# Performance work log

Measured on AMD Instinct MI355X. Metric: run time of the kernel, lower is better.

Reference implementation:

```python
import jax, jax.numpy as jnp
import numpy as np

N, E, G = 10000, 160000, 64     # nodes, edges, graphs in batch
T, F_IN, F_OUT, L = 5, 75, 15, 4  # towers, per-tower in (divide_input=False), per-tower out, conv layers
AVG_DEG_LOG = float(np.log(17.0))  # stand-in for PyG histogram stat (source deg=zeros -> NaN)
BN_EPS = 1e-5
STD_EPS = 1e-5


def _u(key, shape):
    fi, fo = shape[-2], shape[-1]
    lim = float(np.sqrt(6.0 / (fi + fo)))
    return jax.random.uniform(key, shape, jnp.float32, -lim, lim)


def setup_inputs():
    key = jax.random.key(0)
    k = iter(jax.random.split(key, 24))
    inp = {}
    inp["x"] = jax.random.randint(next(k), (N, 2), 0, 21)
    inp["edge_index"] = jax.random.randint(next(k), (2, E), 0, N)
    inp["edge_attr"] = jax.random.randint(next(k), (E, 2), 0, 4)
    inp["batch"] = jnp.sort(jax.random.randint(next(k), (N,), 0, G))
    inp["node_emb"] = jax.random.normal(next(k), (21, 75), jnp.float32)
    inp["edge_emb"] = jax.random.normal(next(k), (4, 25), jnp.float32)
    inp["pre_lin_W"] = _u(next(k), (150, 75)); inp["pre_lin_b"] = jnp.zeros((75,), jnp.float32)
    inp["edge_enc_W"] = _u(next(k), (L, 50, F_IN)); inp["edge_enc_b"] = jnp.zeros((L, F_IN), jnp.float32)
    inp["pre_W"] = _u(next(k), (L, T, 3 * F_IN, F_IN)); inp["pre_b"] = jnp.zeros((L, T, F_IN), jnp.float32)
    inp["post_W"] = _u(next(k), (L, T, 13 * F_IN, F_OUT)); inp["post_b"] = jnp.zeros((L, T, F_OUT), jnp.float32)
    inp["lin_W"] = _u(next(k), (L, T * F_OUT, 75)); inp["lin_b"] = jnp.zeros((L, 75), jnp.float32)
    inp["bn_g"] = jnp.ones((L, 75), jnp.float32); inp["bn_b"] = jnp.zeros((L, 75), jnp.float32)
    inp["mlp_W1"] = _u(next(k), (75, 50)); inp["mlp_b1"] = jnp.zeros((50,), jnp.float32)
    inp["mlp_W2"] = _u(next(k), (50, 25)); inp["mlp_b2"] = jnp.zeros((25,), jnp.float32)
    inp["mlp_W3"] = _u(next(k), (25, 1)); inp["mlp_b3"] = jnp.zeros((1,), jnp.float32)
    return inp


def _forward(x, edge_index, edge_attr, batch, node_emb, edge_emb, pre_lin_W, pre_lin_b,
             edge_enc_W, edge_enc_b, pre_W, pre_b, post_W, post_b, lin_W, lin_b,
             bn_g, bn_b, mlp_W1, mlp_b1, mlp_W2, mlp_b2, mlp_W3, mlp_b3):
    # node / edge embeddings -> features
    h = node_emb[x].reshape(N, 150) @ pre_lin_W + pre_lin_b          # [N,75]
    ea = edge_emb[edge_attr].reshape(E, 50)                           # [E,50]
    src, dst = edge_index[0], edge_index[1]  # messages flow src -> dst (x_j=src, x_i=dst)

    cnt = jax.ops.segment_sum(jnp.ones((E,), jnp.float32), dst, num_segments=N)  # in-degree [N]
    deg = jnp.maximum(cnt, 1.0)[:, None, None]
    log_deg = jnp.log(jnp.maximum(cnt, 1.0) + 1.0)[:, None, None]
    amp = log_deg / AVG_DEG_LOG
    att = AVG_DEG_LOG / log_deg
    has = (cnt > 0)[:, None, None]

    for l in range(L):
        e = ea @ edge_enc_W[l] + edge_enc_b[l]                        # [E,75]
        m_in = jnp.concatenate([h[dst], h[src], e], axis=-1)          # [E,225]
        msgs = jnp.einsum('ec,tcf->etf', m_in, pre_W[l]) + pre_b[l]   # [E,T,75]
        s = jax.ops.segment_sum(msgs, dst, num_segments=N)
        mean = s / deg
        mean_sq = jax.ops.segment_sum(msgs * msgs, dst, num_segments=N) / deg
        std = jnp.sqrt(jax.nn.relu(mean_sq - mean * mean) + STD_EPS)
        mn = jnp.where(has, jax.ops.segment_min(msgs, dst, num_segments=N), 0.0)
        mx = jnp.where(has, jax.ops.segment_max(msgs, dst, num_segments=N), 0.0)
        agg = jnp.concatenate([mean, mn, mx, std], axis=-1)           # [N,T,300]
        scaled = jnp.concatenate([agg, agg * amp, agg * att], axis=-1)  # [N,T,900]
        out = jnp.concatenate([jnp.broadcast_to(h[:, None, :], (N, T, F_IN)), scaled], axis=-1)  # [N,T,975]
        post = jnp.einsum('ntc,tcf->ntf', out, post_W[l]) + post_b[l]  # [N,T,15]
        hc = post.reshape(N, T * F_OUT) @ lin_W[l] + lin_b[l]          # [N,75]
        mu = hc.mean(axis=0)
        var = hc.var(axis=0)  # biased, matches BatchNorm1d training mode
        h = jax.nn.relu((hc - mu) / jnp.sqrt(var + BN_EPS) * bn_g[l] + bn_b[l])

    g = jax.ops.segment_sum(h, batch, num_segments=G)                 # global_add_pool [G,75]
    g = jax.nn.relu(g @ mlp_W1 + mlp_b1)
    g = jax.nn.relu(g @ mlp_W2 + mlp_b2)
    return g @ mlp_W3 + mlp_b3                                        # [G,1]


def reference(x, edge_index, edge_attr, batch, node_emb, edge_emb, pre_lin_W, pre_lin_b,
              edge_enc_W, edge_enc_b, pre_W, pre_b, post_W, post_b, lin_W, lin_b,
              bn_g, bn_b, mlp_W1, mlp_b1, mlp_W2, mlp_b2, mlp_W3, mlp_b3):
    return _forward(x, edge_index, edge_attr, batch, node_emb, edge_emb, pre_lin_W, pre_lin_b,
                    edge_enc_W, edge_enc_b, pre_W, pre_b, post_W, post_b, lin_W, lin_b,
                    bn_g, bn_b, mlp_W1, mlp_b1, mlp_W2, mlp_b2, mlp_W3, mlp_b3)
```

## Files before the change

kernel.cpp:

```cpp
#include <hip/hip_runtime.h>
#include <hip/hip_bf16.h>
#include <math.h>

#define NN 10000
#define NE 160000
#define NG 64
#define NT 5
#define NL 4
#define ADL 2.833213344056216f

#define OFF_H      0
#define OFF_HC     750000
#define OFF_P      1500000
#define OFF_Q      5250000
#define OFF_AGG    9000000
#define OFF_RLUT   24000000
#define OFF_INVDEG 24006000
#define OFF_AMP    24016000
#define OFF_ATT    24026000
#define OFF_STATS  24036000
#define OFF_GPOOL  24036160
#define OFF_INT    24118960

__device__ __forceinline__ float bf2f(__hip_bfloat16 v){ return __bfloat162float(v); }

__global__ void k_zero_cnt(int* cnt){
    int i = blockIdx.x*256 + threadIdx.x;
    if (i < NN) cnt[i] = 0;
}

__global__ __launch_bounds__(256) void k_h0(const int* __restrict__ x,
        const float* __restrict__ node_emb, const float* __restrict__ plW,
        const float* __restrict__ plb, float* __restrict__ h){
    __shared__ float s_emb[21*75];
    __shared__ float s_W[150*75];
    __shared__ float s_b[75];
    int tid = threadIdx.x;
    for (int i = tid; i < 21*75; i += 256) s_emb[i] = node_emb[i];
    for (int i = tid; i < 150*75; i += 256) s_W[i] = plW[i];
    if (tid < 75) s_b[tid] = plb[tid];
    __syncthreads();
    for (int out = blockIdx.x*256 + tid; out < NN*75; out += gridDim.x*256){
        int n = out / 75, f = out - n*75;
        int x0 = x[2*n], x1 = x[2*n+1];
        float acc = s_b[f];
        const float* e0 = s_emb + x0*75;
        const float* e1 = s_emb + x1*75;
        #pragma unroll 5
        for (int k = 0; k < 75; k++)
            acc += e0[k]*s_W[k*75+f] + e1[k]*s_W[(75+k)*75+f];
        h[out] = acc;
    }
}

__global__ void k_hist(const int* __restrict__ ei, int* __restrict__ cnt){
    int e = blockIdx.x*256 + threadIdx.x;
    if (e < NE) atomicAdd(&cnt[ei[NE + e]], 1);
}

__global__ void k_scan(const int* __restrict__ cnt, int* __restrict__ eoff){
    __shared__ int buf[256];
    __shared__ int carry;
    int tid = threadIdx.x;
    if (tid == 0){ carry = 0; eoff[0] = 0; }
    __syncthreads();
    for (int base = 0; base < NN; base += 256){
        int v = (base + tid < NN) ? cnt[base + tid] : 0;
        buf[tid] = v; __syncthreads();
        for (int off = 1; off < 256; off <<= 1){
            int t2 = (tid >= off) ? buf[tid - off] : 0;
            __syncthreads();
            buf[tid] += t2;
            __syncthreads();
        }
        int inc = buf[tid] + carry;
        if (base + tid < NN) eoff[base + tid + 1] = inc;
        __syncthreads();
        if (tid == 255) carry = inc;
        __syncthreads();
    }
}

__global__ void k_nodestats(const int* __restrict__ cnt, const int* __restrict__ eoff,
        float* __restrict__ invdeg, float* __restrict__ amp, float* __restrict__ att,
        int* __restrict__ cursor){
    int n = blockIdx.x*256 + threadIdx.x;
    if (n >= NN) return;
    int c = cnt[n];
    cursor[n] = eoff[n];
    float cf = (float)c;
    float dg = cf < 1.f ? 1.f : cf;
    invdeg[n] = 1.f / dg;
    float ld = logf(dg + 1.f);
    amp[n] = ld / ADL;
    att[n] = ADL / ld;
}

__global__ void k_scatter(const int* __restrict__ ei, const int* __restrict__ ea,
        int* __restrict__ cursor, int* __restrict__ esrc, int* __restrict__ ecombo){
    int e = blockIdx.x*256 + threadIdx.x;
    if (e >= NE) return;
    int src = ei[e], dst = ei[NE + e];
    int pos = atomicAdd(&cursor[dst], 1);
    esrc[pos] = src;
    ecombo[pos] = ea[2*e]*4 + ea[2*e+1];
}

__global__ __launch_bounds__(384) void k_pq(const float* __restrict__ h,
        const float* __restrict__ preW, const float* __restrict__ preb,
        const float* __restrict__ edge_emb, const float* __restrict__ encW,
        const float* __restrict__ encb, int l,
        __hip_bfloat16* __restrict__ P, __hip_bfloat16* __restrict__ Q,
        float* __restrict__ Rlut, float* __restrict__ stats){
    __shared__ float smem[10675];
    int tid = threadIdx.x;
    int bx = blockIdx.x;

    if (bx == 318){
        for (int i = tid; i < 150; i += 384) stats[i] = 0.f;
        return;
    }
    if (bx >= 313){
        int t = bx - 313;
        float* s_encW = smem;
        float* s_ev   = smem + 3750;
        float* s_wc   = smem + 4950;
        float* s_ee   = smem + 10575;
        for (int i = tid; i < 3750; i += 384) s_encW[i] = encW[(size_t)l*3750 + i];
        for (int i = tid; i < 100; i += 384) s_ee[i] = edge_emb[i];
        const float* wcsrc = preW + (((size_t)(l*NT + t))*225 + 150)*75;
        for (int i = tid; i < 5625; i += 384) s_wc[i] = wcsrc[i];
        __syncthreads();
        for (int task = tid; task < 1200; task += 384){
            int b = task/75, m = task - 75*b;
            int a0 = b >> 2, a1 = b & 3;
            float s = encb[l*75 + m];
            for (int k = 0; k < 25; k++)
                s += s_ee[a0*25+k]*s_encW[k*75+m] + s_ee[a1*25+k]*s_encW[(25+k)*75+m];
            s_ev[task] = s;
        }
        __syncthreads();
        for (int task = tid; task < 1200; task += 384){
            int b = task/75, f = task - 75*b;
            float r = preb[((size_t)l*NT + t)*75 + f];
            const float* ev = s_ev + b*75;
            #pragma unroll 5
            for (int m = 0; m < 75; m++) r += ev[m]*s_wc[m*75 + f];
            Rlut[b*375 + t*75 + f] = r;
        }
        return;
    }

    float* h_t = smem;
    int base = bx*32;
    for (int idx = tid; idx < 32*75; idx += 384){
        int i = idx/75, m = idx - 75*i;
        int n = base + i;
        h_t[i*76 + m] = (n < NN) ? h[(size_t)n*75 + m] : 0.f;
    }
    __syncthreads();
    int j = tid;
    if (j >= 375) return;
    int t = j/75, f = j - 75*t;
    const float* wbase = preW + ((size_t)(l*NT + t))*225*75 + f;
    float accP[32], accQ[32];
    #pragma unroll
    for (int i = 0; i < 32; i++){ accP[i] = 0.f; accQ[i] = 0.f; }
    for (int m = 0; m < 72; m += 4){
        float wa0 = wbase[(m+0)*75], wa1 = wbase[(m+1)*75];
        float wa2 = wbase[(m+2)*75], wa3 = wbase[(m+3)*75];
        float wb0 = wbase[(75+m+0)*75], wb1 = wbase[(75+m+1)*75];
        float wb2 = wbase[(75+m+2)*75], wb3 = wbase[(75+m+3)*75];
        #pragma unroll
        for (int i = 0; i < 32; i++){
            const float4 hv = *(const float4*)&h_t[i*76 + m];
            accP[i] += hv.x*wa0 + hv.y*wa1 + hv.z*wa2 + hv.w*wa3;
            accQ[i] += hv.x*wb0 + hv.y*wb1 + hv.z*wb2 + hv.w*wb3;
        }
    }
    for (int m = 72; m < 75; m++){
        float wa = wbase[m*75], wb = wbase[(75+m)*75];
        #pragma unroll
        for (int i = 0; i < 32; i++){
            float v = h_t[i*76 + m];
            accP[i] += v*wa; accQ[i] += v*wb;
        }
    }
    for (int i = 0; i < 32; i++){
        int n = base + i;
        if (n < NN){
            P[(size_t)n*375 + j] = __float2bfloat16(accP[i]);
            Q[(size_t)n*375 + j] = __float2bfloat16(accQ[i]);
        }
    }
}

__global__ __launch_bounds__(64) void k_agg(const __hip_bfloat16* __restrict__ P,
        const __hip_bfloat16* __restrict__ Q, const float* __restrict__ Rlut,
        const int* __restrict__ eoff, const int* __restrict__ esrc,
        const int* __restrict__ ecombo, const float* __restrict__ invdeg,
        __hip_bfloat16* __restrict__ agg){
    int n = blockIdx.y;
    int j = blockIdx.x*64 + threadIdx.x;
    if (j >= 375) return;
    int lo = eoff[n], hi = eoff[n+1];
    float p = bf2f(P[(size_t)n*375 + j]);
    float sum = 0.f, sq = 0.f, mn = 3.4e38f, mx = -3.4e38f;
    int e = lo;
    for (; e + 8 <= hi; e += 8){
        int s0 = esrc[e],   s1 = esrc[e+1], s2 = esrc[e+2], s3 = esrc[e+3];
        int s4 = esrc[e+4], s5 = esrc[e+5], s6 = esrc[e+6], s7 = esrc[e+7];
        int c0 = ecombo[e],   c1 = ecombo[e+1], c2 = ecombo[e+2], c3 = ecombo[e+3];
        int c4 = ecombo[e+4], c5 = ecombo[e+5], c6 = ecombo[e+6], c7 = ecombo[e+7];
        float q0 = bf2f(Q[(size_t)s0*375 + j]);
        float q1 = bf2f(Q[(size_t)s1*375 + j]);
        float q2 = bf2f(Q[(size_t)s2*375 + j]);
        float q3 = bf2f(Q[(size_t)s3*375 + j]);
        float q4 = bf2f(Q[(size_t)s4*375 + j]);
        float q5 = bf2f(Q[(size_t)s5*375 + j]);
        float q6 = bf2f(Q[(size_t)s6*375 + j]);
        float q7 = bf2f(Q[(size_t)s7*375 + j]);
        float r0 = Rlut[c0*375 + j], r1 = Rlut[c1*375 + j];
        float r2 = Rlut[c2*375 + j], r3 = Rlut[c3*375 + j];
        float r4 = Rlut[c4*375 + j], r5 = Rlut[c5*375 + j];
        float r6 = Rlut[c6*375 + j], r7 = Rlut[c7*375 + j];
        float m0 = p + q0 + r0, m1 = p + q1 + r1;
        float m2 = p + q2 + r2, m3 = p + q3 + r3;
        float m4 = p + q4 + r4, m5 = p + q5 + r5;
        float m6 = p + q6 + r6, m7 = p + q7 + r7;
        sum += (m0 + m1 + m2 + m3) + (m4 + m5 + m6 + m7);
        sq  += (m0*m0 + m1*m1 + m2*m2 + m3*m3) + (m4*m4 + m5*m5 + m6*m6 + m7*m7);
        mn = fminf(mn, fminf(fminf(fminf(m0,m1), fminf(m2,m3)),
                             fminf(fminf(m4,m5), fminf(m6,m7))));
        mx = fmaxf(mx, fmaxf(fmaxf(fmaxf(m0,m1), fmaxf(m2,m3)),
                             fmaxf(fmaxf(m4,m5), fmaxf(m6,m7))));
    }
    for (; e < hi; e++){
        int s = esrc[e], cm = ecombo[e];
        float m = p + bf2f(Q[(size_t)s*375 + j]) + Rlut[cm*375 + j];
        sum += m; sq += m*m;
        mn = fminf(mn, m); mx = fmaxf(mx, m);
    }
    float id = invdeg[n];
    bool has = hi > lo;
    float mean = sum*id;
    float msq  = sq*id;
    float var = msq - mean*mean; var = var > 0.f ? var : 0.f;
    float sd = sqrtf(var + 1e-5f);
    float mnv = has ? mn : 0.f;
    float mxv = has ? mx : 0.f;
    int t = j/75, f = j - 75*t;
    __hip_bfloat16* a = agg + ((size_t)n*NT + t)*300;
    a[f]      = __float2bfloat16(mean);
    a[75+f]   = __float2bfloat16(mnv);
    a[150+f]  = __float2bfloat16(mxv);
    a[225+f]  = __float2bfloat16(sd);
}

#define KB2 50
__global__ __launch_bounds__(256, 6) void k_post(const float* __restrict__ h,
        const __hip_bfloat16* __restrict__ agg, const float* __restrict__ postW,
        const float* __restrict__ postb, const float* __restrict__ amp,
        const float* __restrict__ att, int l, float* __restrict__ postbase){
    __shared__ float s_w[3*KB2*16];
    int t = blockIdx.y;
    int z = blockIdx.z;
    int nbase = blockIdx.x*256;
    int tid = threadIdx.x;
    int fg  = (tid & 3)*4;
    int sub = tid >> 2;
    const float* Wt = postW + ((size_t)(l*NT + t))*975*15;

    if (z == 0){
        for (int idx = tid; idx < 75*16; idx += 256){
            int c = idx >> 4, f = idx & 15;
            s_w[idx] = (f < 15) ? Wt[c*15 + f] : 0.f;
        }
        __syncthreads();
        float a1[4][4] = {};
        const float* hrow[4];
        #pragma unroll
        for (int j = 0; j < 4; j++){
            int n = nbase + sub + 64*j;
            hrow[j] = h + (size_t)(n < NN ? n : 0)*75;
        }
        #pragma unroll 3
        for (int k = 0; k < 75; k++){
            const float4 w1 = *(const float4*)&s_w[k*16 + fg];
            #pragma unroll
            for (int j = 0; j < 4; j++){
                float v = hrow[j][k];
                a1[j][0] += v*w1.x; a1[j][1] += v*w1.y;
                a1[j][2] += v*w1.z; a1[j][3] += v*w1.w;
            }
        }
        const float* pb = postb + (l*NT + t)*15;
        #pragma unroll
        for (int j = 0; j < 4; j++){
            int n = nbase + sub + 64*j;
            if (n >= NN) continue;
            float* dst = postbase + (size_t)n*75 + t*15;
            #pragma unroll
            for (int f = 0; f < 4; f++)
                if (fg + f < 15) dst[fg + f] = a1[j][f] + pb[fg + f];
        }
        return;
    }

    int kbeg = (z-1)*KB2;
    for (int idx = tid; idx < 3*KB2*16; idx += 256){
        int vrow = idx / (KB2*16);
        int rem = idx - vrow*(KB2*16);
        int c = rem >> 4, f = rem & 15;
        s_w[idx] = (f < 15) ? Wt[(75 + vrow*300 + kbeg + c)*15 + f] : 0.f;
    }
    __syncthreads();
    float a1[4][4] = {}, a2[4][4] = {}, a3[4][4] = {};
    const __hip_bfloat16* arow[4];
    #pragma unroll
    for (int j = 0; j < 4; j++){
        int n = nbase + sub + 64*j;
        arow[j] = agg + (size_t)(n < NN ? n : 0)*1500 + t*300 + kbeg;
    }
    #pragma unroll 2
    for (int k = 0; k < KB2; k++){
        const float4 w1 = *(const float4*)&s_w[k*16 + fg];
        const float4 w2 = *(const float4*)&s_w[(KB2 + k)*16 + fg];
        const float4 w3 = *(const float4*)&s_w[(2*KB2 + k)*16 + fg];
        #pragma unroll
        for (int j = 0; j < 4; j++){
            float v = bf2f(arow[j][k]);
            a1[j][0] += v*w1.x; a1[j][1] += v*w1.y;
            a1[j][2] += v*w1.z; a1[j][3] += v*w1.w;
            a2[j][0] += v*w2.x; a2[j][1] += v*w2.y;
            a2[j][2] += v*w2.z; a2[j][3] += v*w2.w;
            a3[j][0] += v*w3.x; a3[j][1] += v*w3.y;
            a3[j][2] += v*w3.z; a3[j][3] += v*w3.w;
        }
    }
    float* postv = postbase + (size_t)z*750000;
    #pragma unroll
    for (int j = 0; j < 4; j++){
        int n = nbase + sub + 64*j;
        if (n >= NN) continue;
        float am = amp[n], at = att[n];
        float* dst = postv + (size_t)n*75 + t*15;
        #pragma unroll
        for (int f = 0; f < 4; f++)
            if (fg + f < 15)
                dst[fg + f] = a1[j][f] + am*a2[j][f] + at*a3[j][f];
    }
}

__global__ __launch_bounds__(256) void k_lin(const float* __restrict__ postbase,
        const float* __restrict__ linW, const float* __restrict__ linb,
        int l, float* __restrict__ hc, float* __restrict__ stats){
    __shared__ float p_l[32*75];
    __shared__ float w_l[75*75];
    __shared__ float hc_l[32*75];
    int tid = threadIdx.x;
    int base = blockIdx.x*32;
    for (int i = tid; i < 75*75; i += 256) w_l[i] = linW[(size_t)l*5625 + i];
    for (int i = tid; i < 32*75; i += 256){
        int n = base + i/75;
        size_t idx = (size_t)base*75 + i;
        float v = 0.f;
        if (n < NN){
            #pragma unroll
            for (int z = 0; z < 7; z++) v += postbase[idx + (size_t)z*750000];
        }
        p_l[i] = v;
    }
    __syncthreads();
    for (int task = tid; task < 2400; task += 256){
        int i = task/75, o = task - 75*i;
        float s = linb[l*75 + o];
        const float* pl = p_l + i*75;
        #pragma unroll 5
        for (int j = 0; j < 75; j++) s += pl[j]*w_l[j*75 + o];
        hc_l[task] = s;
        if (base + i < NN) hc[(size_t)(base+i)*75 + o] = s;
    }
    __syncthreads();
    if (tid < 75){
        int nv = NN - base; if (nv > 32) nv = 32;
        float s1 = 0.f, s2 = 0.f;
        for (int i = 0; i < nv; i++){
            float v = hc_l[i*75 + tid];
            s1 += v; s2 += v*v;
        }
        atomicAdd(&stats[tid], s1);
        atomicAdd(&stats[75+tid], s2);
    }
}

__global__ void k_bnapply(const float* __restrict__ hc, const float* __restrict__ stats,
        const float* __restrict__ bng, const float* __restrict__ bnb, int l,
        float* __restrict__ h){
    int idx = blockIdx.x*256 + threadIdx.x;
    if (idx >= NN*75) return;
    int col = idx % 75;
    float mu = stats[col]*(1.0f/NN);
    float var = stats[75+col]*(1.0f/NN) - mu*mu;
    float inv = rsqrtf(var + 1e-5f);
    float v = (hc[idx] - mu)*inv*bng[l*75+col] + bnb[l*75+col];
    h[idx] = v > 0.f ? v : 0.f;
}

__global__ __launch_bounds__(256) void k_pool(const float* __restrict__ h,
        const int* __restrict__ batch, float* __restrict__ gpool){
    int g = blockIdx.x, tid = threadIdx.x;
    int lo = 0, hi = NN;
    while (lo < hi){ int mid = (lo+hi)>>1; if (batch[mid] < g) lo = mid+1; else hi = mid; }
    int start = lo;
    lo = start; hi = NN;
    while (lo < hi){ int mid = (lo+hi)>>1; if (batch[mid] < g+1) lo = mid+1; else hi = mid; }
    int end = lo;
    __shared__ float red[225];
    if (tid < 225){
        int col = tid % 75, rep = tid / 75;
        float acc = 0.f;
        for (int i = start + rep; i < end; i += 3) acc += h[(size_t)i*75 + col];
        red[tid] = acc;
    }
    __syncthreads();
    if (tid < 75) gpool[g*75 + tid] = red[tid] + red[75+tid] + red[150+tid];
}

__global__ __launch_bounds__(256) void k_mlp(const float* __restrict__ gpool,
        const float* __restrict__ W1, const float* __restrict__ b1,
        const float* __restrict__ W2, const float* __restrict__ b2,
        const float* __restrict__ W3, const float* __restrict__ b3,
        float* __restrict__ out){
    __shared__ float w1[75*50];
    __shared__ float w2[50*25];
    __shared__ float gp[8*75];
    __shared__ float t1[8*50];
    __shared__ float t2[8*25];
    int tid = threadIdx.x;
    int gbase = blockIdx.x*8;
    for (int i = tid; i < 75*50; i += 256) w1[i] = W1[i];
    for (int i = tid; i < 50*25; i += 256) w2[i] = W2[i];
    for (int i = tid; i < 8*75; i += 256) gp[i] = gpool[gbase*75 + i];
    __syncthreads();
    for (int task = tid; task < 8*50; task += 256){
        int g = task/50, j = task - 50*g;
        float s = b1[j];
        const float* gv = gp + g*75;
        #pragma unroll 5
        for (int k = 0; k < 75; k++) s += gv[k]*w1[k*50+j];
        t1[task] = s > 0.f ? s : 0.f;
    }
    __syncthreads();
    for (int task = tid; task < 8*25; task += 256){
        int g = task/25, j = task - 25*g;
        float s = b2[j];
        const float* tv = t1 + g*50;
        #pragma unroll 5
        for (int k = 0; k < 50; k++) s += tv[k]*w2[k*25+j];
        t2[task] = s > 0.f ? s : 0.f;
    }
    __syncthreads();
    if (tid < 8){
        float s = b3[0];
        const float* tv = t2 + tid*25;
        #pragma unroll
        for (int k = 0; k < 25; k++) s += tv[k]*W3[k];
        out[gbase + tid] = s;
    }
}

extern "C" void kernel_launch(void* const* d_in, const int* in_sizes, int n_in,
                              void* d_out, int out_size, void* d_ws, size_t ws_size,
                              hipStream_t stream){
    const int* x          = (const int*)d_in[0];
    const int* edge_index = (const int*)d_in[1];
    const int* edge_attr  = (const int*)d_in[2];
    const int* batch      = (const int*)d_in[3];
    const float* node_emb = (const float*)d_in[4];
    const float* edge_emb = (const float*)d_in[5];
    const float* pre_lin_W= (const float*)d_in[6];
    const float* pre_lin_b= (const float*)d_in[7];
    const float* encW     = (const float*)d_in[8];
    const float* encb     = (const float*)d_in[9];
    const float* preW     = (const float*)d_in[10];
    const float* preb     = (const float*)d_in[11];
    const float* postW    = (const float*)d_in[12];
    const float* postb    = (const float*)d_in[13];
    const float* linW     = (const float*)d_in[14];
    const float* linb     = (const float*)d_in[15];
    const float* bng      = (const float*)d_in[16];
    const float* bnb      = (const float*)d_in[17];
    const float* mlpW1    = (const float*)d_in[18];
    const float* mlpb1    = (const float*)d_in[19];
    const float* mlpW2    = (const float*)d_in[20];
    const float* mlpb2    = (const float*)d_in[21];
    const float* mlpW3    = (const float*)d_in[22];
    const float* mlpb3    = (const float*)d_in[23];

    float* ws = (float*)d_ws;
    float* h      = ws + OFF_H;
    float* hc     = ws + OFF_HC;
    __hip_bfloat16* P = (__hip_bfloat16*)(ws + OFF_P);
    __hip_bfloat16* Q = (__hip_bfloat16*)(ws + OFF_Q);
    __hip_bfloat16* agg = (__hip_bfloat16*)(ws + OFF_AGG);
    float* Rlut   = ws + OFF_RLUT;
    float* invdeg = ws + OFF_INVDEG;
    float* amp    = ws + OFF_AMP;
    float* att    = ws + OFF_ATT;
    float* stats  = ws + OFF_STATS;
    float* gpool  = ws + OFF_GPOOL;
    float* postbase = ws + OFF_P;
    int* iw     = (int*)(ws + OFF_INT);
    int* cnt    = iw;
    int* eoff   = cnt + NN;
    int* cursor = eoff + NN + 2;
    int* esrc   = cursor + NN;
    int* ecombo = esrc + NE;

    k_zero_cnt<<<40, 256, 0, stream>>>(cnt);
    k_h0<<<640, 256, 0, stream>>>(x, node_emb, pre_lin_W, pre_lin_b, h);
    k_hist<<<625, 256, 0, stream>>>(edge_index, cnt);
    k_scan<<<1, 256, 0, stream>>>(cnt, eoff);
    k_nodestats<<<40, 256, 0, stream>>>(cnt, eoff, invdeg, amp, att, cursor);
    k_scatter<<<625, 256, 0, stream>>>(edge_index, edge_attr, cursor, esrc, ecombo);

    for (int l = 0; l < NL; l++){
        k_pq<<<319, 384, 0, stream>>>(h, preW, preb, edge_emb, encW, encb, l,
                                      P, Q, Rlut, stats);
        k_agg<<<dim3(6, NN), 64, 0, stream>>>(P, Q, Rlut, eoff, esrc, ecombo, invdeg, agg);
        k_post<<<dim3(40, 5, 7), 256, 0, stream>>>(h, agg, postW, postb, amp, att, l, postbase);
        k_lin<<<313, 256, 0, stream>>>(postbase, linW, linb, l, hc, stats);
        k_bnapply<<<2930, 256, 0, stream>>>(hc, stats, bng, bnb, l, h);
    }

    k_pool<<<NG, 256, 0, stream>>>(h, batch, gpool);
    k_mlp<<<8, 256, 0, stream>>>(gpool, mlpW1, mlpb1, mlpW2, mlpb2, mlpW3, mlpb3, (float*)d_out);
}
```

Baseline: 919.4 us.

## Fold post and lin weights into one bf16 MFMA GEMM per layer

Precomputes a combined weight matrix per layer by multiplying the post-tower weights by the lin weights. Node features are written into a padded bf16 activation row next to the aggregates, so a single MFMA-based GEMM computes the identity, amplification and attenuation branches and also collects BN statistics. This replaces the scalar FP32 k_post, which wrote 7 partial buffers, and the separate k_lin pass. In exchange it adds a weight-prep kernel each layer and more bf16 rounding, since both h and the combined weights are now bf16.

After: 951.3 us. 1.03x slower.

```diff
diff --git a/kernel.cpp b/kernel.cpp
--- a/kernel.cpp
+++ b/kernel.cpp
@@ -8,12 +8,18 @@
 #define NT 5
 #define NL 4
 #define ADL 2.833213344056216f
+#define AROW 1632
+
+typedef __attribute__((ext_vector_type(8))) short bf16x8;
+typedef __attribute__((ext_vector_type(4))) float f32x4;
 
 #define OFF_H      0
 #define OFF_HC     750000
 #define OFF_P      1500000
 #define OFF_Q      5250000
-#define OFF_AGG    9000000
+#define OFF_A      9000000
+#define OFF_BT     17200000
+#define OFF_BIASC  17400000
 #define OFF_RLUT   24000000
 #define OFF_INVDEG 24006000
 #define OFF_AMP    24016000
@@ -29,9 +35,18 @@
     if (i < NN) cnt[i] = 0;
 }
 
+__global__ void k_zpad(__hip_bfloat16* __restrict__ A){
+    int idx = blockIdx.x*256 + threadIdx.x;
+    if (idx >= NN*57) return;
+    int n = idx/57, c = idx - n*57;
+    int k = (c < 36) ? 1500 + c : 1611 + (c - 36);
+    A[(size_t)n*AROW + k] = __float2bfloat16(0.f);
+}
+
 __global__ __launch_bounds__(256) void k_h0(const int* __restrict__ x,
         const float* __restrict__ node_emb, const float* __restrict__ plW,
-        const float* __restrict__ plb, float* __restrict__ h){
+        const float* __restrict__ plb, float* __restrict__ h,
+        __hip_bfloat16* __restrict__ A){
     __shared__ float s_emb[21*75];
     __shared__ float s_W[150*75];
     __shared__ float s_b[75];
@@ -50,6 +65,7 @@
         for (int k = 0; k < 75; k++)
             acc += e0[k]*s_W[k*75+f] + e1[k]*s_W[(75+k)*75+f];
         h[out] = acc;
+        A[(size_t)n*AROW + 1536 + f] = __float2bfloat16(acc);
     }
 }
 
@@ -199,7 +215,7 @@
         const __hip_bfloat16* __restrict__ Q, const float* __restrict__ Rlut,
         const int* __restrict__ eoff, const int* __restrict__ esrc,
         const int* __restrict__ ecombo, const float* __restrict__ invdeg,
-        __hip_bfloat16* __restrict__ agg){
+        __hip_bfloat16* __restrict__ A){
     int n = blockIdx.y;
     int j = blockIdx.x*64 + threadIdx.x;
     if (j >= 375) return;
@@ -250,161 +266,141 @@
     float mnv = has ? mn : 0.f;
     float mxv = has ? mx : 0.f;
     int t = j/75, f = j - 75*t;
-    __hip_bfloat16* a = agg + ((size_t)n*NT + t)*300;
+    __hip_bfloat16* a = A + (size_t)n*AROW + t*300;
     a[f]      = __float2bfloat16(mean);
     a[75+f]   = __float2bfloat16(mnv);
     a[150+f]  = __float2bfloat16(mxv);
     a[225+f]  = __float2bfloat16(sd);
 }
 
-#define KB2 50
-__global__ __launch_bounds__(256, 6) void k_post(const float* __restrict__ h,
-        const __hip_bfloat16* __restrict__ agg, const float* __restrict__ postW,
-        const float* __restrict__ postb, const float* __restrict__ amp,
-        const float* __restrict__ att, int l, float* __restrict__ postbase){
-    __shared__ float s_w[3*KB2*16];
-    int t = blockIdx.y;
-    int z = blockIdx.z;
-    int nbase = blockIdx.x*256;
+__global__ __launch_bounds__(256) void k_prep(const float* __restrict__ postW,
+        const float* __restrict__ postb, const float* __restrict__ linW,
+        const float* __restrict__ linb, int l,
+        __hip_bfloat16* __restrict__ BT, float* __restrict__ biasc){
     int tid = threadIdx.x;
-    int fg  = (tid & 3)*4;
-    int sub = tid >> 2;
-    const float* Wt = postW + ((size_t)(l*NT + t))*975*15;
-
-    if (z == 0){
-        for (int idx = tid; idx < 75*16; idx += 256){
-            int c = idx >> 4, f = idx & 15;
-            s_w[idx] = (f < 15) ? Wt[c*15 + f] : 0.f;
-        }
+    if (blockIdx.x == 1530){
+        if (tid < 80){
+            float s = (tid < 75) ? linb[l*75 + tid] : 0.f;
+            if (tid < 75)
+                for (int tf = 0; tf < 75; tf++)
+                    s += postb[l*75 + tf]*linW[(size_t)l*5625 + tf*75 + tid];
+            biasc[tid] = s;
+        }
+        return;
+    }
+    __shared__ float s_lin[5625];
+    for (int i = tid; i < 5625; i += 256) s_lin[i] = linW[(size_t)l*5625 + i];
+    __syncthreads();
+    int idx = blockIdx.x*256 + tid;
+    int mat = idx / (80*AROW);
+    int rem = idx - mat*(80*AROW);
+    int o = rem / AROW;
+    int k = rem - o*AROW;
+    float v = 0.f;
+    if (o < 75){
+        if (k < 1500){
+            int t = k / 300, kk = k - t*300;
+            int c = (mat == 0 ? 75 : (mat == 1 ? 375 : 675)) + kk;
+            const float* pw = postW + (((size_t)(l*NT + t))*975 + c)*15;
+            const float* lw = s_lin + t*15*75 + o;
+            #pragma unroll
+            for (int f = 0; f < 15; f++) v += pw[f]*lw[f*75];
+        } else if (k >= 1536 && k < 1611 && mat == 0){
+            int c = k - 1536;
+            for (int t = 0; t < 5; t++){
+                const float* pw = postW + (((size_t)(l*NT + t))*975 + c)*15;
+                const float* lw = s_lin + t*15*75 + o;
+                #pragma unroll
+                for (int f = 0; f < 15; f++) v += pw[f]*lw[f*75];
+            }
+        }
+    }
+    BT[idx] = __float2bfloat16(v);
+}
+
+__global__ __launch_bounds__(256) void k_gemm(const __hip_bfloat16* __restrict__ A,
+        const __hip_bfloat16* __restrict__ BT, const float* __restrict__ biasc,
+        const float* __restrict__ amp, const float* __restrict__ att,
+        float* __restrict__ hc, float* __restrict__ stats){
+    __shared__ float scratch[4*16*80];
+    __shared__ float comb[3*16*80];
+    int tid = threadIdx.x;
+    int wave = tid >> 6;
+    int lane = tid & 63;
+    int nb = blockIdx.x;
+    int mrow = lane & 15;
+    int q = lane >> 4;
+    int n0 = nb*16;
+
+    f32x4 acc[3][5];
+    #pragma unroll
+    for (int mt = 0; mt < 3; mt++)
+        #pragma unroll
+        for (int nt = 0; nt < 5; nt++)
+            acc[mt][nt] = (f32x4){0.f, 0.f, 0.f, 0.f};
+
+    int k0 = wave*13;
+    int k1 = (wave == 3) ? 51 : k0 + 13;
+    const __hip_bfloat16* arow_p = A + (size_t)(n0 + mrow)*AROW + q*8;
+    for (int ks = k0; ks < k1; ks++){
+        bf16x8 afrag = *(const bf16x8*)(arow_p + (size_t)ks*32);
+        #pragma unroll
+        for (int mt = 0; mt < 3; mt++){
+            const __hip_bfloat16* bbase = BT + ((size_t)mt*80 + mrow)*AROW + q*8 + (size_t)ks*32;
+            #pragma unroll
+            for (int nt = 0; nt < 5; nt++){
+                bf16x8 bfrag = *(const bf16x8*)(bbase + (size_t)nt*16*AROW);
+                acc[mt][nt] = __builtin_amdgcn_mfma_f32_16x16x32_bf16(
+                                  afrag, bfrag, acc[mt][nt], 0, 0, 0);
+            }
+        }
+    }
+    for (int mt = 0; mt < 3; mt++){
+        #pragma unroll
+        for (int nt = 0; nt < 5; nt++)
+            #pragma unroll
+            for (int r = 0; r < 4; r++)
+                scratch[(wave*16 + q*4 + r)*80 + nt*16 + (lane & 15)] = acc[mt][nt][r];
         __syncthreads();
-        float a1[4][4] = {};
-        const float* hrow[4];
-        #pragma unroll
-        for (int j = 0; j < 4; j++){
-            int n = nbase + sub + 64*j;
-            hrow[j] = h + (size_t)(n < NN ? n : 0)*75;
-        }
-        #pragma unroll 3
-        for (int k = 0; k < 75; k++){
-            const float4 w1 = *(const float4*)&s_w[k*16 + fg];
-            #pragma unroll
-            for (int j = 0; j < 4; j++){
-                float v = hrow[j][k];
-                a1[j][0] += v*w1.x; a1[j][1] += v*w1.y;
-                a1[j][2] += v*w1.z; a1[j][3] += v*w1.w;
-            }
-        }
-        const float* pb = postb + (l*NT + t)*15;
-        #pragma unroll
-        for (int j = 0; j < 4; j++){
-            int n = nbase + sub + 64*j;
-            if (n >= NN) continue;
-            float* dst = postbase + (size_t)n*75 + t*15;
-            #pragma unroll
-            for (int f = 0; f < 4; f++)
-                if (fg + f < 15) dst[fg + f] = a1[j][f] + pb[fg + f];
-        }
-        return;
-    }
-
-    int kbeg = (z-1)*KB2;
-    for (int idx = tid; idx < 3*KB2*16; idx += 256){
-        int vrow = idx / (KB2*16);
-        int rem = idx - vrow*(KB2*16);
-        int c = rem >> 4, f = rem & 15;
-        s_w[idx] = (f < 15) ? Wt[(75 + vrow*300 + kbeg + c)*15 + f] : 0.f;
-    }
-    __syncthreads();
-    float a1[4][4] = {}, a2[4][4] = {}, a3[4][4] = {};
-    const __hip_bfloat16* arow[4];
-    #pragma unroll
-    for (int j = 0; j < 4; j++){
-        int n = nbase + sub + 64*j;
-        arow[j] = agg + (size_t)(n < NN ? n : 0)*1500 + t*300 + kbeg;
-    }
-    #pragma unroll 2
-    for (int k = 0; k < KB2; k++){
-        const float4 w1 = *(const float4*)&s_w[k*16 + fg];
-        const float4 w2 = *(const float4*)&s_w[(KB2 + k)*16 + fg];
-        const float4 w3 = *(const float4*)&s_w[(2*KB2 + k)*16 + fg];
-        #pragma unroll
-        for (int j = 0; j < 4; j++){
-            float v = bf2f(arow[j][k]);
-            a1[j][0] += v*w1.x; a1[j][1] += v*w1.y;
-            a1[j][2] += v*w1.z; a1[j][3] += v*w1.w;
-            a2[j][0] += v*w2.x; a2[j][1] += v*w2.y;
-            a2[j][2] += v*w2.z; a2[j][3] += v*w2.w;
-            a3[j][0] += v*w3.x; a3[j][1] += v*w3.y;
-            a3[j][2] += v*w3.z; a3[j][3] += v*w3.w;
-        }
-    }
-    float* postv = postbase + (size_t)z*750000;
-    #pragma unroll
-    for (int j = 0; j < 4; j++){
-        int n = nbase + sub + 64*j;
-        if (n >= NN) continue;
-        float am = amp[n], at = att[n];
-        float* dst = postv + (size_t)n*75 + t*15;
-        #pragma unroll
-        for (int f = 0; f < 4; f++)
-            if (fg + f < 15)
-                dst[fg + f] = a1[j][f] + am*a2[j][f] + at*a3[j][f];
-    }
-}
-
-__global__ __launch_bounds__(256) void k_lin(const float* __restrict__ postbase,
-        const float* __restrict__ linW, const float* __restrict__ linb,
-        int l, float* __restrict__ hc, float* __restrict__ stats){
-    __shared__ float p_l[32*75];
-    __shared__ float w_l[75*75];
-    __shared__ float hc_l[32*75];
-    int tid = threadIdx.x;
-    int base = blockIdx.x*32;
-    for (int i = tid; i < 75*75; i += 256) w_l[i] = linW[(size_t)l*5625 + i];
-    for (int i = tid; i < 32*75; i += 256){
-        int n = base + i/75;
-        size_t idx = (size_t)base*75 + i;
-        float v = 0.f;
-        if (n < NN){
-            #pragma unroll
-            for (int z = 0; z < 7; z++) v += postbase[idx + (size_t)z*750000];
-        }
-        p_l[i] = v;
-    }
-    __syncthreads();
-    for (int task = tid; task < 2400; task += 256){
-        int i = task/75, o = task - 75*i;
-        float s = linb[l*75 + o];
-        const float* pl = p_l + i*75;
-        #pragma unroll 5
-        for (int j = 0; j < 75; j++) s += pl[j]*w_l[j*75 + o];
-        hc_l[task] = s;
-        if (base + i < NN) hc[(size_t)(base+i)*75 + o] = s;
+        for (int i = tid; i < 16*80; i += 256)
+            comb[mt*1280 + i] = scratch[i] + scratch[1280 + i]
+                              + scratch[2560 + i] + scratch[3840 + i];
+        __syncthreads();
+    }
+    for (int i = tid; i < 16*80; i += 256){
+        int r = i / 80, o = i - r*80;
+        int n = n0 + r;
+        float v = comb[i] + amp[n]*comb[1280 + i] + att[n]*comb[2560 + i] + biasc[o];
+        scratch[i] = v;
+        if (o < 75) hc[(size_t)n*75 + o] = v;
     }
     __syncthreads();
     if (tid < 75){
-        int nv = NN - base; if (nv > 32) nv = 32;
         float s1 = 0.f, s2 = 0.f;
-        for (int i = 0; i < nv; i++){
-            float v = hc_l[i*75 + tid];
+        #pragma unroll
+        for (int r = 0; r < 16; r++){
+            float v = scratch[r*80 + tid];
             s1 += v; s2 += v*v;
         }
         atomicAdd(&stats[tid], s1);
-        atomicAdd(&stats[75+tid], s2);
+        atomicAdd(&stats[75 + tid], s2);
     }
 }
 
 __global__ void k_bnapply(const float* __restrict__ hc, const float* __restrict__ stats,
         const float* __restrict__ bng, const float* __restrict__ bnb, int l,
-        float* __restrict__ h){
+        float* __restrict__ h, __hip_bfloat16* __restrict__ A){
     int idx = blockIdx.x*256 + threadIdx.x;
     if (idx >= NN*75) return;
     int col = idx % 75;
+    int n = idx / 75;
     float mu = stats[col]*(1.0f/NN);
     float var = stats[75+col]*(1.0f/NN) - mu*mu;
     float inv = rsqrtf(var + 1e-5f);
     float v = (hc[idx] - mu)*inv*bng[l*75+col] + bnb[l*75+col];
-    h[idx] = v > 0.f ? v : 0.f;
+    v = v > 0.f ? v : 0.f;
+    h[idx] = v;
+    A[(size_t)n*AROW + 1536 + col] = __float2bfloat16(v);
 }
 
 __global__ __launch_bounds__(256) void k_pool(const float* __restrict__ h,
@@ -503,14 +499,15 @@
     float* hc     = ws + OFF_HC;
     __hip_bfloat16* P = (__hip_bfloat16*)(ws + OFF_P);
     __hip_bfloat16* Q = (__hip_bfloat16*)(ws + OFF_Q);
-    __hip_bfloat16* agg = (__hip_bfloat16*)(ws + OFF_AGG);
+    __hip_bfloat16* A = (__hip_bfloat16*)(ws + OFF_A);
+    __hip_bfloat16* BT = (__hip_bfloat16*)(ws + OFF_BT);
+    float* biasc  = ws + OFF_BIASC;
     float* Rlut   = ws + OFF_RLUT;
     float* invdeg = ws + OFF_INVDEG;
     float* amp    = ws + OFF_AMP;
     float* att    = ws + OFF_ATT;
     float* stats  = ws + OFF_STATS;
     float* gpool  = ws + OFF_GPOOL;
-    float* postbase = ws + OFF_P;
     int* iw     = (int*)(ws + OFF_INT);
     int* cnt    = iw;
     int* eoff   = cnt + NN;
@@ -519,7 +516,8 @@
     int* ecombo = esrc + NE;
 
     k_zero_cnt<<<40, 256, 0, stream>>>(cnt);
-    k_h0<<<640, 256, 0, stream>>>(x, node_emb, pre_lin_W, pre_lin_b, h);
+    k_zpad<<<(NN*57 + 255)/256, 256, 0, stream>>>(A);
+    k_h0<<<640, 256, 0, stream>>>(x, node_emb, pre_lin_W, pre_lin_b, h, A);
     k_hist<<<625, 256, 0, stream>>>(edge_index, cnt);
     k_scan<<<1, 256, 0, stream>>>(cnt, eoff);
     k_nodestats<<<40, 256, 0, stream>>>(cnt, eoff, invdeg, amp, att, cursor);
@@ -528,10 +526,10 @@
     for (int l = 0; l < NL; l++){
         k_pq<<<319, 384, 0, stream>>>(h, preW, preb, edge_emb, encW, encb, l,
                                       P, Q, Rlut, stats);
-        k_agg<<<dim3(6, NN), 64, 0, stream>>>(P, Q, Rlut, eoff, esrc, ecombo, invdeg, agg);
-        k_post<<<dim3(40, 5, 7), 256, 0, stream>>>(h, agg, postW, postb, amp, att, l, postbase);
-        k_lin<<<313, 256, 0, stream>>>(postbase, linW, linb, l, hc, stats);
-        k_bnapply<<<2930, 256, 0, stream>>>(hc, stats, bng, bnb, l, h);
+        k_agg<<<dim3(6, NN), 64, 0, stream>>>(P, Q, Rlut, eoff, esrc, ecombo, invdeg, A);
+        k_prep<<<1531, 256, 0, stream>>>(postW, postb, linW, linb, l, BT, biasc);
+        k_gemm<<<625, 256, 0, stream>>>(A, BT, biasc, amp, att, hc, stats);
+        k_bnapply<<<2930, 256, 0, stream>>>(hc, stats, bng, bnb, l, h, A);
     }
 
     k_pool<<<NG, 256, 0, stream>>>(h, batch, gpool);
```
